# Kernel optimization log

Hardware: AMD Instinct MI355X
Metric: run time of the kernel (lower is better)

The kernel has to match this reference:

```python
import jax, jax.numpy as jnp
import numpy as np

EPS = 1e-6
GROUPS = 32


def group_norm(x, scale, bias):
    # x: [b, c, d, h, w]
    b, c, d, h, w = x.shape
    xg = x.reshape(b, GROUPS, c // GROUPS, d, h, w)
    mean = xg.mean(axis=(2, 3, 4, 5), keepdims=True)
    var = xg.var(axis=(2, 3, 4, 5), keepdims=True)
    xn = ((xg - mean) * jax.lax.rsqrt(var + EPS)).reshape(b, c, d, h, w)
    return xn * scale[None, :, None, None, None] + bias[None, :, None, None, None]


def setup_inputs() -> dict:
    key = jax.random.key(0)
    ks = jax.random.split(key, 6)
    C = 512
    x = jax.random.normal(ks[0], (2, C, 16, 16, 16), dtype=jnp.float32)
    s = 1.0 / np.sqrt(C)
    return {
        "x": x,
        "gn_scale": jnp.ones((C,), jnp.float32),
        "gn_bias": jnp.zeros((C,), jnp.float32),
        "wq": jax.random.normal(ks[1], (C, C), jnp.float32) * s,
        "bq": jnp.zeros((C,), jnp.float32),
        "wk": jax.random.normal(ks[2], (C, C), jnp.float32) * s,
        "bk": jnp.zeros((C,), jnp.float32),
        "wv": jax.random.normal(ks[3], (C, C), jnp.float32) * s,
        "bv": jnp.zeros((C,), jnp.float32),
        "wproj": jax.random.normal(ks[4], (C, C), jnp.float32) * s,
        "bproj": jnp.zeros((C,), jnp.float32),
    }


def reference(x, gn_scale, gn_bias, wq, bq, wk, bk, wv, bv, wproj, bproj):
    b, c, d, h, w = x.shape
    h_ = group_norm(x, gn_scale, gn_bias)
    hf = h_.reshape(b, c, d * h * w)  # [b, c, N]
    # 1x1x1 convs == per-position channel matmuls
    q = jnp.einsum("oc,bcn->bon", wq, hf) + bq[None, :, None]
    k = jnp.einsum("oc,bcn->bon", wk, hf) + bk[None, :, None]
    v = jnp.einsum("oc,bcn->bon", wv, hf) + bv[None, :, None]
    # attn[b, i, j] = softmax_j(q_i . k_j / sqrt(c))
    attn = jnp.einsum("bci,bcj->bij", q, k) * (c ** -0.5)
    attn = jax.nn.softmax(attn, axis=-1)
    # out[b, c, i] = sum_j v[b, c, j] * attn[b, i, j]
    out = jnp.einsum("bcj,bij->bci", v, attn)
    out = jnp.einsum("oc,bcn->bon", wproj, out) + bproj[None, :, None]
    return x + out.reshape(b, c, d, h, w)
```

## Files before the change

kernel.cpp:

```cpp
#include <hip/hip_runtime.h>
#include <hip/hip_bf16.h>

#define BB 2
#define CC 512
#define GG 32
#define NN 4096
#define EPSV 1e-6f

typedef __attribute__((ext_vector_type(4))) float f32x4;
typedef __attribute__((ext_vector_type(8))) short s16x8;
typedef __attribute__((ext_vector_type(4))) short s16x4;

__device__ __forceinline__ ushort f2bf(float f){
  union { float f; unsigned u; } v; v.f = f;
  unsigned r = v.u + 0x7fffu + ((v.u >> 16) & 1u);
  return (ushort)(r >> 16);
}
__device__ __forceinline__ short f2bfs(float f){ return (short)f2bf(f); }
__device__ __forceinline__ float b2f(ushort u){
  union { unsigned u; float f; } v; v.u = ((unsigned)u) << 16; return v.f;
}

__device__ __forceinline__ f32x4 mfma16(s16x8 a, s16x8 b, f32x4 c){
  return __builtin_amdgcn_mfma_f32_16x16x32_bf16(a, b, c, 0, 0, 0);
}

#define GLOAD_LDS16(g, l) __builtin_amdgcn_global_load_lds( \
    (const __attribute__((address_space(1))) void*)(g),     \
    (__attribute__((address_space(3))) void*)(l), 16, 0, 0)

__global__ __launch_bounds__(256) void k_convert_w(const float* __restrict__ wq, const float* __restrict__ wk,
                                                   const float* __restrict__ wv, const float* __restrict__ wp,
                                                   ushort* __restrict__ wbf){
  int idx = blockIdx.x * 256 + threadIdx.x;
  const float* srcs[4] = {wq, wk, wv, wp};
  #pragma unroll
  for (int m = 0; m < 4; m++){
    float4 v = reinterpret_cast<const float4*>(srcs[m])[idx];
    ushort4 o; o.x = f2bf(v.x); o.y = f2bf(v.y); o.z = f2bf(v.z); o.w = f2bf(v.w);
    reinterpret_cast<ushort4*>(wbf + (size_t)m * CC * CC)[idx] = o;
  }
}

__global__ __launch_bounds__(256) void k_gn_stats1(const float* __restrict__ x, float* __restrict__ pstat){
  int blk = blockIdx.x;
  const float* p = x + (size_t)blk * 16384;
  float s = 0.f, ss = 0.f;
  for (int i = threadIdx.x; i < 4096; i += 256){
    float4 v = reinterpret_cast<const float4*>(p)[i];
    s  += v.x + v.y + v.z + v.w;
    ss += v.x*v.x + v.y*v.y + v.z*v.z + v.w*v.w;
  }
  #pragma unroll
  for (int off = 32; off; off >>= 1){ s += __shfl_down(s, off); ss += __shfl_down(ss, off); }
  __shared__ float rs_[4], rss_[4];
  int w = threadIdx.x >> 6, lane = threadIdx.x & 63;
  if (lane == 0){ rs_[w] = s; rss_[w] = ss; }
  __syncthreads();
  if (threadIdx.x == 0){
    pstat[blk * 2 + 0] = rs_[0] + rs_[1] + rs_[2] + rs_[3];
    pstat[blk * 2 + 1] = rss_[0] + rss_[1] + rss_[2] + rss_[3];
  }
}
__global__ __launch_bounds__(64) void k_gn_stats2(const float* __restrict__ pstat, float* __restrict__ stats){
  int bg = blockIdx.x;
  int l = threadIdx.x;
  float s = 0.f, ss = 0.f;
  if (l < 4){ s = pstat[(bg * 4 + l) * 2]; ss = pstat[(bg * 4 + l) * 2 + 1]; }
  #pragma unroll
  for (int off = 2; off; off >>= 1){ s += __shfl_down(s, off); ss += __shfl_down(ss, off); }
  if (l == 0){
    float inv = 1.0f / (16.0f * NN);
    float mean = s * inv;
    float var = ss * inv - mean * mean;
    stats[bg * 2 + 0] = mean;
    stats[bg * 2 + 1] = rsqrtf(var + EPSV);
  }
}

__global__ __launch_bounds__(256) void k_gn_apply(const float* __restrict__ x, const float* __restrict__ gsc,
                                                  const float* __restrict__ gbi, const float* __restrict__ stats,
                                                  ushort* __restrict__ hf){
  __shared__ ushort tr[32][520];
  int b = blockIdx.y;
  int nb = blockIdx.x * 32;
  int t = threadIdx.x;
  int n = t & 31, cr = t >> 5;
  const float* xb = x + (size_t)b * CC * NN;
  for (int c0 = 0; c0 < CC; c0 += 8){
    int c = c0 + cr;
    float mean = stats[(b * GG + (c >> 4)) * 2 + 0];
    float rstd = stats[(b * GG + (c >> 4)) * 2 + 1];
    float v = xb[(size_t)c * NN + nb + n];
    tr[n][c] = f2bf((v - mean) * rstd * gsc[c] + gbi[c]);
  }
  __syncthreads();
  ushort* out = hf + ((size_t)b * NN + nb) * CC;
  int c8 = (t & 63) * 8;
  int nrow0 = t >> 6;
  #pragma unroll
  for (int i = 0; i < 8; i++){
    int nr = nrow0 + i * 4;
    *reinterpret_cast<s16x8*>(&out[(size_t)nr * CC + c8]) =
      *reinterpret_cast<const s16x8*>(&tr[nr][c8]);
  }
}

__global__ __launch_bounds__(256, 3) void k_gemm_qkv2(const ushort* __restrict__ W, const ushort* __restrict__ Bt,
                                                      const float* __restrict__ bq, const float* __restrict__ bk,
                                                      const float* __restrict__ bv,
                                                      ushort* __restrict__ qo, ushort* __restrict__ ko,
                                                      ushort* __restrict__ vo, float rs){
  __shared__ __align__(16) char smem[40960];
  __shared__ float bl[3][64];
  int b = blockIdx.z, ob = blockIdx.y * 64, nb = blockIdx.x * 128;
  int t = threadIdx.x, w = t >> 6, l = t & 63;
  int lr = l & 15, lk = l >> 4;
  int wo = (w >> 1) * 32, wn = (w & 1) * 64;
  if (t < 64){ bl[0][t] = bq[ob + t]; bl[1][t] = bk[ob + t]; bl[2][t] = bv[ob + t]; }
  const ushort* Bp = Bt + ((size_t)b * NN + nb) * CC;
  const ushort* Wp = W + (size_t)ob * CC;
  int srow = l >> 2;
  int schunk = (l & 3) ^ ((l >> 2) & 3) ^ ((l >> 4) & 3);
  int xs = (lk ^ (lr & 3) ^ ((lr >> 2) & 3)) * 8;

#define STAGE_QKV(BUF, K0)                                                               \
  {                                                                                      \
    ushort* As_ = (ushort*)(smem + (BUF) * 20480);                                       \
    ushort* Bs_ = As_ + 6144;                                                            \
    _Pragma("unroll")                                                                    \
    for (int tt = 0; tt < 5; tt++){                                                      \
      int inst = w * 5 + tt;                                                             \
      if (inst < 12){                                                                    \
        int m = inst >> 2, sub = inst & 3;                                               \
        const ushort* src = Wp + (size_t)m * CC * CC + (size_t)(sub * 16 + srow) * CC + (K0) + schunk * 8; \
        GLOAD_LDS16(src, As_ + m * 2048 + sub * 512);                                    \
      } else {                                                                           \
        int q = inst - 12;                                                               \
        const ushort* src = Bp + (size_t)(q * 16 + srow) * CC + (K0) + schunk * 8;       \
        GLOAD_LDS16(src, Bs_ + q * 512);                                                 \
      }                                                                                  \
    }                                                                                    \
  }

  f32x4 acc[3][2][4] = {};
  STAGE_QKV(0, 0)
  __syncthreads();
  for (int s16 = 0; s16 < 16; s16++){
    if (s16 < 15) STAGE_QKV((s16 + 1) & 1, (s16 + 1) * 32)
    const ushort* As = (const ushort*)(smem + (s16 & 1) * 20480);
    const ushort* Bs = As + 6144;
    s16x8 bf[4];
    #pragma unroll
    for (int sn = 0; sn < 4; sn++)
      bf[sn] = *(const s16x8*)&Bs[(wn + sn * 16 + lr) * 32 + xs];
    #pragma unroll
    for (int m = 0; m < 3; m++){
      s16x8 a0 = *(const s16x8*)&As[m * 2048 + (wo + lr) * 32 + xs];
      s16x8 a1 = *(const s16x8*)&As[m * 2048 + (wo + 16 + lr) * 32 + xs];
      #pragma unroll
      for (int sn = 0; sn < 4; sn++){
        acc[m][0][sn] = mfma16(a0, bf[sn], acc[m][0][sn]);
        acc[m][1][sn] = mfma16(a1, bf[sn], acc[m][1][sn]);
      }
    }
    __syncthreads();
  }
#undef STAGE_QKV
  #pragma unroll
  for (int m = 0; m < 2; m++){
    ushort* dst = (m == 0) ? qo : ko;
    float scl = (m == 0) ? rs : 1.0f;
    #pragma unroll
    for (int so = 0; so < 2; so++)
      #pragma unroll
      for (int sn = 0; sn < 4; sn++){
        int o0 = wo + so * 16 + lk * 4;
        int n  = nb + wn + sn * 16 + lr;
        s16x4 pv;
        #pragma unroll
        for (int r = 0; r < 4; r++) pv[r] = f2bfs((acc[m][so][sn][r] + bl[m][o0 + r]) * scl);
        *reinterpret_cast<s16x4*>(&dst[((size_t)b * NN + n) * CC + ob + o0]) = pv;
      }
  }
  ushort* Ve = (ushort*)smem;
  #pragma unroll
  for (int so = 0; so < 2; so++)
    #pragma unroll
    for (int sn = 0; sn < 4; sn++){
      int o0 = wo + so * 16 + lk * 4;
      int ncl = wn + sn * 16 + lr;
      #pragma unroll
      for (int r = 0; r < 4; r++) Ve[(o0 + r) * 136 + ncl] = f2bf(acc[2][so][sn][r] + bl[2][o0 + r]);
    }
  __syncthreads();
  {
    int row = t >> 2, cs = (t & 3) * 32;
    ushort* dst = &vo[((size_t)b * CC + ob + row) * NN + nb + cs];
    #pragma unroll
    for (int k = 0; k < 4; k++)
      *(s16x8*)&dst[k * 8] = *(const s16x8*)&Ve[row * 136 + cs + k * 8];
  }
}

__global__ __launch_bounds__(512, 2) void k_gemm_s(const ushort* __restrict__ qt, const ushort* __restrict__ kt,
                                                   ushort* __restrict__ P, float* __restrict__ part){
  extern __shared__ __align__(16) char smem[];
  int lin = blockIdx.x + 16 * blockIdx.y + 256 * blockIdx.z;
  int tt0 = (lin & 7) * 64 + (lin >> 3);
  int jblk = tt0 & 15;
  int pair = tt0 >> 4;
  int b = pair >> 4;
  int j0 = jblk * 256, i0 = (pair & 15) * 256;
  int t = threadIdx.x, w = t >> 6, l = t & 63;
  int lr = l & 15, lk = l >> 4;
  int wj2 = w >> 2, wi4 = w & 3;
  const ushort* kb = kt + ((size_t)b * NN + j0) * CC;
  const ushort* qb = qt + ((size_t)b * NN + i0) * CC;
  int srow = l >> 3;
  int schunk = (l & 7) ^ srow;

#define STAGE_KH(BUF, K0, H)                                                      \
  {                                                                               \
    ushort* D = (ushort*)(smem + (BUF) * 32768);                                  \
    _Pragma("unroll")                                                             \
    for (int tt = 0; tt < 2; tt++){                                               \
      int g = (H) * 16 + w * 2 + tt;                                              \
      const ushort* src = kb + (size_t)(g * 8 + srow) * CC + (K0) + schunk * 8;   \
      GLOAD_LDS16(src, D + g * 512);                                              \
    }                                                                             \
  }
#define STAGE_QH(BUF, K0, H)                                                      \
  {                                                                               \
    ushort* D = (ushort*)(smem + 65536 + (BUF) * 32768);                          \
    _Pragma("unroll")                                                             \
    for (int tt = 0; tt < 2; tt++){                                               \
      int g = (H) * 16 + w * 2 + tt;                                              \
      const ushort* src = qb + (size_t)(g * 8 + srow) * CC + (K0) + schunk * 8;   \
      GLOAD_LDS16(src, D + g * 512);                                              \
    }                                                                             \
  }
#define PHASE(SJ, STAGE_CODE)                                                     \
  {                                                                               \
    s16x8 a00 = *(const s16x8*)&Ks[(wj2 * 128 + (SJ) * 16 + lr) * 64 + xs0];      \
    s16x8 a01 = *(const s16x8*)&Ks[(wj2 * 128 + (SJ) * 16 + lr) * 64 + xs1];      \
    s16x8 a10 = *(const s16x8*)&Ks[(wj2 * 128 + ((SJ) + 1) * 16 + lr) * 64 + xs0];\
    s16x8 a11 = *(const s16x8*)&Ks[(wj2 * 128 + ((SJ) + 1) * 16 + lr) * 64 + xs1];\
    STAGE_CODE                                                                    \
    __builtin_amdgcn_s_barrier();                                                 \
    asm volatile("s_waitcnt lgkmcnt(0)" ::: "memory");                            \
    __builtin_amdgcn_sched_barrier(0);                                            \
    __builtin_amdgcn_s_setprio(1);                                                \
    _Pragma("unroll")                                                             \
    for (int si = 0; si < 4; si++){                                               \
      acc[SJ][si]       = mfma16(a00, bq[si][0], acc[SJ][si]);                    \
      acc[SJ][si]       = mfma16(a01, bq[si][1], acc[SJ][si]);                    \
      acc[(SJ) + 1][si] = mfma16(a10, bq[si][0], acc[(SJ) + 1][si]);              \
      acc[(SJ) + 1][si] = mfma16(a11, bq[si][1], acc[(SJ) + 1][si]);              \
    }                                                                             \
    __builtin_amdgcn_s_setprio(0);                                                \
    __builtin_amdgcn_s_barrier();                                                 \
  }

  f32x4 acc[8][4] = {};
  STAGE_KH(0, 0, 0)
  STAGE_KH(0, 0, 1)
  STAGE_QH(0, 0, 0)
  STAGE_QH(0, 0, 1)
  STAGE_QH(1, 64, 0)
  STAGE_QH(1, 64, 1)
  #pragma unroll
  for (int s8 = 0; s8 < 8; s8++){
    const int tau = s8 & 1;
    const ushort* Ks = (const ushort*)(smem + tau * 32768);
    const ushort* Qs = (const ushort*)(smem + 65536 + tau * 32768);
    if (s8 < 7){ asm volatile("s_waitcnt vmcnt(4)" ::: "memory"); }
    else       { asm volatile("s_waitcnt vmcnt(0)" ::: "memory"); }
    __builtin_amdgcn_s_barrier();
    __builtin_amdgcn_sched_barrier(0);
    int xs0 = (lk ^ (lr & 7)) * 8;
    int xs1 = ((4 + lk) ^ (lr & 7)) * 8;
    s16x8 bq[4][2];
    #pragma unroll
    for (int si = 0; si < 4; si++){
      bq[si][0] = *(const s16x8*)&Qs[(wi4 * 64 + si * 16 + lr) * 64 + xs0];
      bq[si][1] = *(const s16x8*)&Qs[(wi4 * 64 + si * 16 + lr) * 64 + xs1];
    }
    PHASE(0, if (s8 < 7) STAGE_KH(tau ^ 1, (s8 + 1) * 64, 0))
    PHASE(2, if (s8 < 7) STAGE_KH(tau ^ 1, (s8 + 1) * 64, 1))
    PHASE(4, if (s8 < 6) STAGE_QH(tau, (s8 + 2) * 64, 0))
    PHASE(6, if (s8 < 6) STAGE_QH(tau, (s8 + 2) * 64, 1))
  }
#undef PHASE
#undef STAGE_KH
#undef STAGE_QH
  ushort* Pe = (ushort*)smem;
  float rsum[4] = {0.f, 0.f, 0.f, 0.f};
  #pragma unroll
  for (int pass = 0; pass < 2; pass++){
    if ((wi4 >> 1) == pass){
      #pragma unroll
      for (int sj = 0; sj < 8; sj++)
        #pragma unroll
        for (int si = 0; si < 4; si++){
          int il = (wi4 & 1) * 64 + si * 16 + lr;
          int jl = wj2 * 128 + sj * 16 + lk * 4;
          s16x4 pk;
          #pragma unroll
          for (int r = 0; r < 4; r++){
            float e = __builtin_amdgcn_exp2f(acc[sj][si][r]);
            pk[r] = f2bfs(e);
            rsum[si] += e;
          }
          *(s16x4*)&Pe[il * 264 + jl] = pk;
        }
    }
    __syncthreads();
    {
      int row = t >> 2, cs = (t & 3) * 64;
      ushort* dst = P + ((size_t)b * NN + i0 + pass * 128 + row) * NN + j0 + cs;
      #pragma unroll
      for (int k = 0; k < 8; k++)
        *(s16x8*)&dst[k * 8] = *(const s16x8*)&Pe[row * 264 + cs + k * 8];
    }
    __syncthreads();
  }
  #pragma unroll
  for (int si = 0; si < 4; si++){
    float s = rsum[si];
    s += __shfl_xor(s, 16);
    s += __shfl_xor(s, 32);
    if (lk == 0){
      int il = wi4 * 64 + si * 16 + lr;
      part[((size_t)b * NN + i0 + il) * 32 + jblk * 2 + wj2] = s;
    }
  }
}

__global__ __launch_bounds__(256) void k_rowsum2(const float* __restrict__ part, float* __restrict__ linv){
  int row = blockIdx.x * 4 + (threadIdx.x >> 6);
  int l = threadIdx.x & 63;
  float s = (l < 32) ? part[(size_t)row * 32 + l] : 0.f;
  #pragma unroll
  for (int off = 32; off; off >>= 1) s += __shfl_down(s, off);
  if (l == 0) linv[row] = 1.0f / s;
}

__global__ __launch_bounds__(512) void k_gemm_o(const ushort* __restrict__ P, const ushort* __restrict__ vv,
                                                const float* __restrict__ linv, ushort* __restrict__ ot){
  __shared__ __align__(16) char smem[65536];
  int lin = blockIdx.x + 4 * blockIdx.y + 128 * blockIdx.z;
  int tt0 = (lin & 7) * 32 + (lin >> 3);
  int cblk = tt0 & 3;
  int ib   = tt0 >> 2;
  int b = ib >> 5;
  int c0 = cblk * 128, i0 = (ib & 31) * 128;
  int t = threadIdx.x, w = t >> 6, l = t & 63;
  int lr = l & 15, lk = l >> 4;
  int wi2 = w >> 2, wc4 = w & 3;
  const ushort* vb = vv + ((size_t)b * CC + c0) * NN;
  const ushort* pb = P + ((size_t)b * NN + i0) * NN;
  int srow = l >> 3;
  int schunk = (l & 7) ^ srow;

#define STAGE_O(BUF, K0)                                                          \
  {                                                                               \
    ushort* Vs_ = (ushort*)(smem + (BUF) * 16384);                                \
    ushort* Ps_ = (ushort*)(smem + 32768 + (BUF) * 16384);                        \
    _Pragma("unroll")                                                             \
    for (int tt = 0; tt < 4; tt++){                                               \
      int inst = w * 4 + tt;                                                      \
      if (inst < 16){                                                             \
        const ushort* src = vb + (size_t)(inst * 8 + srow) * NN + (K0) + schunk * 8; \
        GLOAD_LDS16(src, Vs_ + inst * 512);                                       \
      } else {                                                                    \
        int g = inst - 16;                                                        \
        const ushort* src = pb + (size_t)(g * 8 + srow) * NN + (K0) + schunk * 8; \
        GLOAD_LDS16(src, Ps_ + g * 512);                                          \
      }                                                                           \
    }                                                                             \
  }

  f32x4 acc[2][4] = {};
  STAGE_O(0, 0)
  for (int s64 = 0; s64 < 64; s64++){
    if (s64 < 63){
      STAGE_O((s64 + 1) & 1, (s64 + 1) * 64)
      asm volatile("s_waitcnt vmcnt(4)" ::: "memory");
    } else {
      asm volatile("s_waitcnt vmcnt(0)" ::: "memory");
    }
    __builtin_amdgcn_s_barrier();
    __builtin_amdgcn_sched_barrier(0);
    const ushort* Vs = (const ushort*)(smem + (s64 & 1) * 16384);
    const ushort* Ps = (const ushort*)(smem + 32768 + (s64 & 1) * 16384);
    #pragma unroll
    for (int kk = 0; kk < 2; kk++){
      int xs = ((kk * 4 + lk) ^ (lr & 7)) * 8;
      s16x8 af[2], bf[4];
      #pragma unroll
      for (int sc = 0; sc < 2; sc++)
        af[sc] = *(const s16x8*)&Vs[(wc4 * 32 + sc * 16 + lr) * 64 + xs];
      #pragma unroll
      for (int si = 0; si < 4; si++)
        bf[si] = *(const s16x8*)&Ps[(wi2 * 64 + si * 16 + lr) * 64 + xs];
      #pragma unroll
      for (int sc = 0; sc < 2; sc++)
        #pragma unroll
        for (int si = 0; si < 4; si++)
          acc[sc][si] = mfma16(af[sc], bf[si], acc[sc][si]);
    }
    asm volatile("s_waitcnt lgkmcnt(0)" ::: "memory");
    __builtin_amdgcn_s_barrier();
    __builtin_amdgcn_sched_barrier(0);
  }
#undef STAGE_O
  ushort* Oe = (ushort*)smem;
  #pragma unroll
  for (int si = 0; si < 4; si++){
    int il = wi2 * 64 + si * 16 + lr;
    float li = linv[(size_t)b * NN + i0 + il];
    #pragma unroll
    for (int sc = 0; sc < 2; sc++){
      int cl = wc4 * 32 + sc * 16 + lk * 4;
      s16x4 pk;
      #pragma unroll
      for (int r = 0; r < 4; r++) pk[r] = f2bfs(acc[sc][si][r] * li);
      *(s16x4*)&Oe[il * 136 + cl] = pk;
    }
  }
  __syncthreads();
  {
    int row = t >> 2, cs = (t & 3) * 32;
    ushort* dst = ot + ((size_t)b * NN + i0 + row) * CC + c0 + cs;
    #pragma unroll
    for (int k = 0; k < 4; k++)
      *(s16x8*)&dst[k * 8] = *(const s16x8*)&Oe[row * 136 + cs + k * 8];
  }
}

__global__ __launch_bounds__(256, 3) void k_gemm_proj2(const ushort* __restrict__ A, const ushort* __restrict__ Bt,
                                                       const float* __restrict__ bias, float* __restrict__ o32,
                                                       const float* __restrict__ xres){
  __shared__ __align__(16) char smem[34048];
  __shared__ float bl[64];
  int b = blockIdx.z, ob = blockIdx.y * 64, nb = blockIdx.x * 128;
  int t = threadIdx.x, w = t >> 6, l = t & 63;
  int lr = l & 15, lk = l >> 4;
  int wo = (w >> 1) * 32, wn = (w & 1) * 64;
  if (t < 64) bl[t] = bias[ob + t];
  const ushort* Bp = Bt + ((size_t)b * NN + nb) * CC;
  const ushort* Ap = A + (size_t)ob * CC;
  int srow = l >> 2;
  int schunk = (l & 3) ^ ((l >> 2) & 3) ^ ((l >> 4) & 3);
  int xs = (lk ^ (lr & 3) ^ ((lr >> 2) & 3)) * 8;

#define STAGE_P2(BUF, K0)                                                         \
  {                                                                               \
    ushort* As_ = (ushort*)(smem + (BUF) * 12288);                                \
    ushort* Bs_ = As_ + 2048;                                                     \
    _Pragma("unroll")                                                             \
    for (int tt = 0; tt < 3; tt++){                                               \
      int inst = w * 3 + tt;                                                      \
      if (inst < 4){                                                              \
        const ushort* src = Ap + (size_t)(inst * 16 + srow) * CC + (K0) + schunk * 8; \
        GLOAD_LDS16(src, As_ + inst * 512);                                       \
      } else {                                                                    \
        int q = inst - 4;                                                         \
        const ushort* src = Bp + (size_t)(q * 16 + srow) * CC + (K0) + schunk * 8; \
        GLOAD_LDS16(src, Bs_ + q * 512);                                          \
      }                                                                           \
    }                                                                             \
  }

  f32x4 acc[2][4] = {};
  STAGE_P2(0, 0)
  __syncthreads();
  for (int s16 = 0; s16 < 16; s16++){
    if (s16 < 15) STAGE_P2((s16 + 1) & 1, (s16 + 1) * 32)
    const ushort* As = (const ushort*)(smem + (s16 & 1) * 12288);
    const ushort* Bs = As + 2048;
    s16x8 a0 = *(const s16x8*)&As[(wo + lr) * 32 + xs];
    s16x8 a1 = *(const s16x8*)&As[(wo + 16 + lr) * 32 + xs];
    #pragma unroll
    for (int sn = 0; sn < 4; sn++){
      s16x8 bf = *(const s16x8*)&Bs[(wn + sn * 16 + lr) * 32 + xs];
      acc[0][sn] = mfma16(a0, bf, acc[0][sn]);
      acc[1][sn] = mfma16(a1, bf, acc[1][sn]);
    }
    __syncthreads();
  }
#undef STAGE_P2
  float* trf = (float*)smem;
  #pragma unroll
  for (int so = 0; so < 2; so++)
    #pragma unroll
    for (int sn = 0; sn < 4; sn++){
      int o0 = wo + so * 16 + lk * 4;
      int ncl = wn + sn * 16 + lr;
      #pragma unroll
      for (int r = 0; r < 4; r++) trf[(o0 + r) * 133 + ncl] = acc[so][sn][r] + bl[o0 + r];
    }
  __syncthreads();
  {
    int row = t >> 2, cs = (t & 3) * 32;
    size_t base = ((size_t)b * CC + ob + row) * NN + nb + cs;
    #pragma unroll
    for (int q = 0; q < 8; q++){
      float4 xv = *reinterpret_cast<const float4*>(&xres[base + q * 4]);
      float4 ov;
      ov.x = xv.x + trf[row * 133 + cs + q * 4 + 0];
      ov.y = xv.y + trf[row * 133 + cs + q * 4 + 1];
      ov.z = xv.z + trf[row * 133 + cs + q * 4 + 2];
      ov.w = xv.w + trf[row * 133 + cs + q * 4 + 3];
      *reinterpret_cast<float4*>(&o32[base + q * 4]) = ov;
    }
  }
}

extern "C" void kernel_launch(void* const* d_in, const int* in_sizes, int n_in,
                              void* d_out, int out_size, void* d_ws, size_t ws_size,
                              hipStream_t stream){
  const float* x   = (const float*)d_in[0];
  const float* gsc = (const float*)d_in[1];
  const float* gbi = (const float*)d_in[2];
  const float* wq  = (const float*)d_in[3];
  const float* bq  = (const float*)d_in[4];
  const float* wk  = (const float*)d_in[5];
  const float* bk  = (const float*)d_in[6];
  const float* wv  = (const float*)d_in[7];
  const float* bv  = (const float*)d_in[8];
  const float* wp  = (const float*)d_in[9];
  const float* bp  = (const float*)d_in[10];
  char* ws = (char*)d_ws;
  const size_t MB = 1024 * 1024;
  ushort* wbf  = (ushort*)ws;
  ushort* qtb  = (ushort*)(ws + 2 * MB);
  ushort* ktb  = (ushort*)(ws + 10 * MB);
  ushort* vvb  = (ushort*)(ws + 18 * MB);
  ushort* hfb  = (ushort*)(ws + 26 * MB);
  ushort* Pbuf = (ushort*)(ws + 34 * MB);
  float* linv  = (float*)(ws + 98 * MB);
  float* stats = (float*)(ws + 98 * MB + 64 * 1024);
  float* pstat = (float*)(ws + 98 * MB + 96 * 1024);
  float* part  = (float*)(ws + 26 * MB);
  ushort* otb = hfb;

  const float rs = 0.044194173824159216f * 1.4426950408889634f;

  k_convert_w<<<256, 256, 0, stream>>>(wq, wk, wv, wp, wbf);
  k_gn_stats1<<<256, 256, 0, stream>>>(x, pstat);
  k_gn_stats2<<<64, 64, 0, stream>>>(pstat, stats);
  k_gn_apply<<<dim3(128, 2, 1), 256, 0, stream>>>(x, gsc, gbi, stats, hfb);
  k_gemm_qkv2<<<dim3(32, 8, 2), 256, 0, stream>>>(wbf, hfb, bq, bk, bv, qtb, ktb, vvb, rs);
  k_gemm_s<<<dim3(16, 16, 2), 512, 131072, stream>>>(qtb, ktb, Pbuf, part);
  k_rowsum2<<<2048, 256, 0, stream>>>(part, linv);
  k_gemm_o<<<dim3(4, 32, 2), 512, 0, stream>>>(Pbuf, vvb, linv, otb);
  k_gemm_proj2<<<dim3(32, 8, 2), 256, 0, stream>>>(wbf + 3 * CC * CC, otb, bp, (float*)d_out, x);
}
```

Before: 180.6 us.

## Fuse prep kernels, fold rowsum into PV GEMM, re-pipeline P·V staging

```diff
diff --git a/kernel.cpp b/kernel.cpp
--- a/kernel.cpp
+++ b/kernel.cpp
@@ -29,20 +29,21 @@
     (const __attribute__((address_space(1))) void*)(g),     \
     (__attribute__((address_space(3))) void*)(l), 16, 0, 0)
 
-__global__ __launch_bounds__(256) void k_convert_w(const float* __restrict__ wq, const float* __restrict__ wk,
-                                                   const float* __restrict__ wv, const float* __restrict__ wp,
-                                                   ushort* __restrict__ wbf){
-  int idx = blockIdx.x * 256 + threadIdx.x;
-  const float* srcs[4] = {wq, wk, wv, wp};
-  #pragma unroll
-  for (int m = 0; m < 4; m++){
-    float4 v = reinterpret_cast<const float4*>(srcs[m])[idx];
-    ushort4 o; o.x = f2bf(v.x); o.y = f2bf(v.y); o.z = f2bf(v.z); o.w = f2bf(v.w);
-    reinterpret_cast<ushort4*>(wbf + (size_t)m * CC * CC)[idx] = o;
-  }
-}
-
-__global__ __launch_bounds__(256) void k_gn_stats1(const float* __restrict__ x, float* __restrict__ pstat){
+__global__ __launch_bounds__(256) void k_prep(const float* __restrict__ wq, const float* __restrict__ wk,
+                                              const float* __restrict__ wv, const float* __restrict__ wp,
+                                              ushort* __restrict__ wbf,
+                                              const float* __restrict__ x, float* __restrict__ pstat){
+  if (blockIdx.x >= 256){
+    int idx = (blockIdx.x - 256) * 256 + threadIdx.x;
+    const float* srcs[4] = {wq, wk, wv, wp};
+    #pragma unroll
+    for (int m = 0; m < 4; m++){
+      float4 v = reinterpret_cast<const float4*>(srcs[m])[idx];
+      ushort4 o; o.x = f2bf(v.x); o.y = f2bf(v.y); o.z = f2bf(v.z); o.w = f2bf(v.w);
+      reinterpret_cast<ushort4*>(wbf + (size_t)m * CC * CC)[idx] = o;
+    }
+    return;
+  }
   int blk = blockIdx.x;
   const float* p = x + (size_t)blk * 16384;
   float s = 0.f, ss = 0.f;
@@ -62,35 +63,35 @@
     pstat[blk * 2 + 1] = rss_[0] + rss_[1] + rss_[2] + rss_[3];
   }
 }
-__global__ __launch_bounds__(64) void k_gn_stats2(const float* __restrict__ pstat, float* __restrict__ stats){
-  int bg = blockIdx.x;
-  int l = threadIdx.x;
-  float s = 0.f, ss = 0.f;
-  if (l < 4){ s = pstat[(bg * 4 + l) * 2]; ss = pstat[(bg * 4 + l) * 2 + 1]; }
-  #pragma unroll
-  for (int off = 2; off; off >>= 1){ s += __shfl_down(s, off); ss += __shfl_down(ss, off); }
-  if (l == 0){
+
+__global__ __launch_bounds__(256) void k_gn_apply(const float* __restrict__ x, const float* __restrict__ gsc,
+                                                  const float* __restrict__ gbi, const float* __restrict__ pstat,
+                                                  ushort* __restrict__ hf){
+  __shared__ ushort tr[32][520];
+  __shared__ float stl[64];
+  int b = blockIdx.y;
+  int nb = blockIdx.x * 32;
+  int t = threadIdx.x;
+  if (t < 32){
+    float s = 0.f, ss = 0.f;
+    #pragma unroll
+    for (int k = 0; k < 4; k++){
+      s  += pstat[(b * 128 + t * 4 + k) * 2 + 0];
+      ss += pstat[(b * 128 + t * 4 + k) * 2 + 1];
+    }
     float inv = 1.0f / (16.0f * NN);
     float mean = s * inv;
     float var = ss * inv - mean * mean;
-    stats[bg * 2 + 0] = mean;
-    stats[bg * 2 + 1] = rsqrtf(var + EPSV);
-  }
-}
-
-__global__ __launch_bounds__(256) void k_gn_apply(const float* __restrict__ x, const float* __restrict__ gsc,
-                                                  const float* __restrict__ gbi, const float* __restrict__ stats,
-                                                  ushort* __restrict__ hf){
-  __shared__ ushort tr[32][520];
-  int b = blockIdx.y;
-  int nb = blockIdx.x * 32;
-  int t = threadIdx.x;
+    stl[t * 2 + 0] = mean;
+    stl[t * 2 + 1] = rsqrtf(var + EPSV);
+  }
+  __syncthreads();
   int n = t & 31, cr = t >> 5;
   const float* xb = x + (size_t)b * CC * NN;
   for (int c0 = 0; c0 < CC; c0 += 8){
     int c = c0 + cr;
-    float mean = stats[(b * GG + (c >> 4)) * 2 + 0];
-    float rstd = stats[(b * GG + (c >> 4)) * 2 + 1];
+    float mean = stl[(c >> 4) * 2 + 0];
+    float rstd = stl[(c >> 4) * 2 + 1];
     float v = xb[(size_t)c * NN + nb + n];
     tr[n][c] = f2bf((v - mean) * rstd * gsc[c] + gbi[c]);
   }
@@ -337,17 +338,8 @@
   }
 }
 
-__global__ __launch_bounds__(256) void k_rowsum2(const float* __restrict__ part, float* __restrict__ linv){
-  int row = blockIdx.x * 4 + (threadIdx.x >> 6);
-  int l = threadIdx.x & 63;
-  float s = (l < 32) ? part[(size_t)row * 32 + l] : 0.f;
-  #pragma unroll
-  for (int off = 32; off; off >>= 1) s += __shfl_down(s, off);
-  if (l == 0) linv[row] = 1.0f / s;
-}
-
 __global__ __launch_bounds__(512) void k_gemm_o(const ushort* __restrict__ P, const ushort* __restrict__ vv,
-                                                const float* __restrict__ linv, ushort* __restrict__ ot){
+                                                const float* __restrict__ part, ushort* __restrict__ ot){
   __shared__ __align__(16) char smem[65536];
   int lin = blockIdx.x + 4 * blockIdx.y + 128 * blockIdx.z;
   int tt0 = (lin & 7) * 32 + (lin >> 3);
@@ -363,63 +355,96 @@
   int srow = l >> 3;
   int schunk = (l & 7) ^ srow;
 
-#define STAGE_O(BUF, K0)                                                          \
+#define STAGE_V(BUF, K0)                                                          \
   {                                                                               \
-    ushort* Vs_ = (ushort*)(smem + (BUF) * 16384);                                \
-    ushort* Ps_ = (ushort*)(smem + 32768 + (BUF) * 16384);                        \
+    ushort* D = (ushort*)(smem + (BUF) * 16384);                                  \
     _Pragma("unroll")                                                             \
-    for (int tt = 0; tt < 4; tt++){                                               \
-      int inst = w * 4 + tt;                                                      \
-      if (inst < 16){                                                             \
-        const ushort* src = vb + (size_t)(inst * 8 + srow) * NN + (K0) + schunk * 8; \
-        GLOAD_LDS16(src, Vs_ + inst * 512);                                       \
-      } else {                                                                    \
-        int g = inst - 16;                                                        \
-        const ushort* src = pb + (size_t)(g * 8 + srow) * NN + (K0) + schunk * 8; \
-        GLOAD_LDS16(src, Ps_ + g * 512);                                          \
-      }                                                                           \
+    for (int tt = 0; tt < 2; tt++){                                               \
+      int g = w * 2 + tt;                                                         \
+      const ushort* src = vb + (size_t)(g * 8 + srow) * NN + (K0) + schunk * 8;   \
+      GLOAD_LDS16(src, D + g * 512);                                              \
     }                                                                             \
   }
+#define STAGE_P(BUF, K0)                                                          \
+  {                                                                               \
+    ushort* D = (ushort*)(smem + 32768 + (BUF) * 16384);                          \
+    _Pragma("unroll")                                                             \
+    for (int tt = 0; tt < 2; tt++){                                               \
+      int g = w * 2 + tt;                                                         \
+      const ushort* src = pb + (size_t)(g * 8 + srow) * NN + (K0) + schunk * 8;   \
+      GLOAD_LDS16(src, D + g * 512);                                              \
+    }                                                                             \
+  }
 
   f32x4 acc[2][4] = {};
-  STAGE_O(0, 0)
+  STAGE_V(0, 0)
+  STAGE_P(0, 0)
+  STAGE_P(1, 64)
   for (int s64 = 0; s64 < 64; s64++){
-    if (s64 < 63){
-      STAGE_O((s64 + 1) & 1, (s64 + 1) * 64)
-      asm volatile("s_waitcnt vmcnt(4)" ::: "memory");
-    } else {
-      asm volatile("s_waitcnt vmcnt(0)" ::: "memory");
-    }
+    const int tau = s64 & 1;
+    const ushort* Vs = (const ushort*)(smem + tau * 16384);
+    const ushort* Ps = (const ushort*)(smem + 32768 + tau * 16384);
+    if (s64 < 63){ asm volatile("s_waitcnt vmcnt(2)" ::: "memory"); }
+    else         { asm volatile("s_waitcnt vmcnt(0)" ::: "memory"); }
     __builtin_amdgcn_s_barrier();
     __builtin_amdgcn_sched_barrier(0);
-    const ushort* Vs = (const ushort*)(smem + (s64 & 1) * 16384);
-    const ushort* Ps = (const ushort*)(smem + 32768 + (s64 & 1) * 16384);
-    #pragma unroll
-    for (int kk = 0; kk < 2; kk++){
-      int xs = ((kk * 4 + lk) ^ (lr & 7)) * 8;
-      s16x8 af[2], bf[4];
-      #pragma unroll
-      for (int sc = 0; sc < 2; sc++)
-        af[sc] = *(const s16x8*)&Vs[(wc4 * 32 + sc * 16 + lr) * 64 + xs];
-      #pragma unroll
-      for (int si = 0; si < 4; si++)
-        bf[si] = *(const s16x8*)&Ps[(wi2 * 64 + si * 16 + lr) * 64 + xs];
-      #pragma unroll
-      for (int sc = 0; sc < 2; sc++)
-        #pragma unroll
-        for (int si = 0; si < 4; si++)
-          acc[sc][si] = mfma16(af[sc], bf[si], acc[sc][si]);
-    }
-    asm volatile("s_waitcnt lgkmcnt(0)" ::: "memory");
-    __builtin_amdgcn_s_barrier();
-    __builtin_amdgcn_sched_barrier(0);
-  }
-#undef STAGE_O
+    int xs0 = (lk ^ (lr & 7)) * 8;
+    int xs1 = ((4 + lk) ^ (lr & 7)) * 8;
+    s16x8 bf[4][2];
+    #pragma unroll
+    for (int si = 0; si < 4; si++){
+      bf[si][0] = *(const s16x8*)&Ps[(wi2 * 64 + si * 16 + lr) * 64 + xs0];
+      bf[si][1] = *(const s16x8*)&Ps[(wi2 * 64 + si * 16 + lr) * 64 + xs1];
+    }
+    {
+      s16x8 af0 = *(const s16x8*)&Vs[(wc4 * 32 + lr) * 64 + xs0];
+      s16x8 af1 = *(const s16x8*)&Vs[(wc4 * 32 + 16 + lr) * 64 + xs0];
+      if (s64 < 63) STAGE_V(tau ^ 1, (s64 + 1) * 64)
+      __builtin_amdgcn_s_barrier();
+      asm volatile("s_waitcnt lgkmcnt(0)" ::: "memory");
+      __builtin_amdgcn_sched_barrier(0);
+      __builtin_amdgcn_s_setprio(1);
+      #pragma unroll
+      for (int si = 0; si < 4; si++){
+        acc[0][si] = mfma16(af0, bf[si][0], acc[0][si]);
+        acc[1][si] = mfma16(af1, bf[si][0], acc[1][si]);
+      }
+      __builtin_amdgcn_s_setprio(0);
+      __builtin_amdgcn_s_barrier();
+    }
+    {
+      s16x8 af0 = *(const s16x8*)&Vs[(wc4 * 32 + lr) * 64 + xs1];
+      s16x8 af1 = *(const s16x8*)&Vs[(wc4 * 32 + 16 + lr) * 64 + xs1];
+      if (s64 < 62) STAGE_P(tau, (s64 + 2) * 64)
+      __builtin_amdgcn_s_barrier();
+      asm volatile("s_waitcnt lgkmcnt(0)" ::: "memory");
+      __builtin_amdgcn_sched_barrier(0);
+      __builtin_amdgcn_s_setprio(1);
+      #pragma unroll
+      for (int si = 0; si < 4; si++){
+        acc[0][si] = mfma16(af0, bf[si][1], acc[0][si]);
+        acc[1][si] = mfma16(af1, bf[si][1], acc[1][si]);
+      }
+      __builtin_amdgcn_s_setprio(0);
+      __builtin_amdgcn_s_barrier();
+    }
+  }
+#undef STAGE_V
+#undef STAGE_P
   ushort* Oe = (ushort*)smem;
+  float* linv_lds = (float*)(smem + 34816);
+  if (t < 128){
+    const float* pp = part + ((size_t)b * NN + i0 + t) * 32;
+    float s = 0.f;
+    #pragma unroll
+    for (int k = 0; k < 32; k++) s += pp[k];
+    linv_lds[t] = 1.0f / s;
+  }
+  __syncthreads();
   #pragma unroll
   for (int si = 0; si < 4; si++){
     int il = wi2 * 64 + si * 16 + lr;
-    float li = linv[(size_t)b * NN + i0 + il];
+    float li = linv_lds[il];
     #pragma unroll
     for (int sc = 0; sc < 2; sc++){
       int cl = wc4 * 32 + sc * 16 + lk * 4;
@@ -540,21 +565,16 @@
   ushort* vvb  = (ushort*)(ws + 18 * MB);
   ushort* hfb  = (ushort*)(ws + 26 * MB);
   ushort* Pbuf = (ushort*)(ws + 34 * MB);
-  float* linv  = (float*)(ws + 98 * MB);
-  float* stats = (float*)(ws + 98 * MB + 64 * 1024);
-  float* pstat = (float*)(ws + 98 * MB + 96 * 1024);
+  float* pstat = (float*)(ws + 98 * MB);
   float* part  = (float*)(ws + 26 * MB);
-  ushort* otb = hfb;
+  ushort* otb  = qtb;
 
   const float rs = 0.044194173824159216f * 1.4426950408889634f;
 
-  k_convert_w<<<256, 256, 0, stream>>>(wq, wk, wv, wp, wbf);
-  k_gn_stats1<<<256, 256, 0, stream>>>(x, pstat);
-  k_gn_stats2<<<64, 64, 0, stream>>>(pstat, stats);
-  k_gn_apply<<<dim3(128, 2, 1), 256, 0, stream>>>(x, gsc, gbi, stats, hfb);
+  k_prep<<<512, 256, 0, stream>>>(wq, wk, wv, wp, wbf, x, pstat);
+  k_gn_apply<<<dim3(128, 2, 1), 256, 0, stream>>>(x, gsc, gbi, pstat, hfb);
   k_gemm_qkv2<<<dim3(32, 8, 2), 256, 0, stream>>>(wbf, hfb, bq, bk, bv, qtb, ktb, vvb, rs);
   k_gemm_s<<<dim3(16, 16, 2), 512, 131072, stream>>>(qtb, ktb, Pbuf, part);
-  k_rowsum2<<<2048, 256, 0, stream>>>(part, linv);
-  k_gemm_o<<<dim3(4, 32, 2), 512, 0, stream>>>(Pbuf, vvb, linv, otb);
+  k_gemm_o<<<dim3(4, 32, 2), 512, 0, stream>>>(Pbuf, vvb, part, otb);
   k_gemm_proj2<<<dim3(32, 8, 2), 256, 0, stream>>>(wbf + 3 * CC * CC, otb, bp, (float*)d_out, x);
 }
```

Measured after the change: 166.2 us, median of 4. 1.09x faster.
